# Performance work log

Measured on AMD Instinct MI355X. Metric: run time of the kernel, lower is better.

The kernel has to match this reference:

```python
import jax, jax.numpy as jnp
import numpy as np

B, L, IN = 8, 128, 64
H, C, A, HEADS = 800, 800, 128, 8
F = IN + H + 6          # states + inputs + angles(3) + distances(3)
RADIUS = 8.0
BOND = 3.8              # CA-CA virtual bond length (Angstrom)


def setup_inputs() -> dict:
    key = jax.random.key(0)
    ks = jax.random.split(key, 8)
    s = 0.05
    return {
        "data": jax.random.normal(ks[0], (B, L, IN), jnp.float32),
        # GRUCell (torch gate order r, z, n)
        "W_ih": jax.random.normal(ks[1], (IN + C, 3 * H), jnp.float32) * s,
        "W_hh": jax.random.normal(ks[2], (H, 3 * H), jnp.float32) * s,
        "b_ih": jnp.zeros((3 * H,), jnp.float32),
        "b_hh": jnp.zeros((3 * H,), jnp.float32),
        # AngleProject: hidden -> 3 torsion angles
        "Wa": jax.random.normal(ks[3], (H, 3), jnp.float32) * s,
        "ba": jnp.zeros((3,), jnp.float32),
        # MILAttention: tanh(x W1) W2 -> per-head logits; head-pooled feats -> context
        "W1": jax.random.normal(ks[4], (F, A), jnp.float32) * s,
        "b1": jnp.zeros((A,), jnp.float32),
        "W2": jax.random.normal(ks[5], (A, HEADS), jnp.float32) * s,
        "Wout": jax.random.normal(ks[6], (HEADS * F, C), jnp.float32) * s,
        "bout": jnp.zeros((C,), jnp.float32),
    }


def _gru(x, h, W_ih, W_hh, b_ih, b_hh):
    gx = x @ W_ih + b_ih
    gh = h @ W_hh + b_hh
    xr, xz, xn = jnp.split(gx, 3, axis=-1)
    hr, hz, hn = jnp.split(gh, 3, axis=-1)
    r = jax.nn.sigmoid(xr + hr)
    z = jax.nn.sigmoid(xz + hz)
    n = jnp.tanh(xn + r * hn)
    return (1.0 - z) * n + z * h


def _forward(data, W_ih, W_hh, b_ih, b_hh, Wa, ba, W1, b1, W2, Wout, bout):
    jpos = jnp.arange(L)

    def step(carry, idx):
        state, context, results, angles, positions = carry
        x = jnp.concatenate([data[:, idx, :], context], axis=-1)        # [B, IN+C]
        state = _gru(x, state, W_ih, W_hh, b_ih, b_hh)                  # [B, H]
        angle = state @ Wa + ba                                         # [B, 3]
        prev = jnp.where(idx > 0, positions[:, idx - 1], 0.0)           # [B, 3, 3]
        # LocalPositionLookup: extend backbone by BOND along angle-derived dirs
        asum = jnp.sum(angle, axis=-1, keepdims=True)
        dirs = jnp.stack([jnp.cos(angle),
                          jnp.sin(angle) * jnp.cos(asum),
                          jnp.sin(angle) * jnp.sin(asum)], axis=-1)     # [B, 3, 3]
        tert = prev + BOND * dirs
        results = results.at[:, idx].set(state)
        angles = angles.at[:, idx].set(angle)
        positions = positions.at[:, idx].set(tert)
        # collect_context: neighbors = {j < idx : ||CA_j - CA_{idx-1}|| <= radius}
        diff = prev[:, None, :, :] - positions                          # [B, L, 3, 3]
        dist = jnp.sqrt(jnp.sum(diff * diff, axis=-1) + 1e-12)          # [B, L, 3]
        mask = (jpos[None, :] < idx) & (dist[:, :, 1] <= RADIUS)        # [B, L]
        feats = jnp.concatenate([results, data, angles, dist], axis=-1)  # [B, L, F]
        # MIL attention pooling per chain (bag = neighbor set)
        e = jnp.tanh(feats @ W1 + b1)                                   # [B, L, A]
        logits = jnp.where(mask[:, :, None], e @ W2, -1e9)              # [B, L, HEADS]
        attn = jax.nn.softmax(logits, axis=1)
        pooled = jnp.einsum('blh,blf->bhf', attn, feats).reshape(B, HEADS * F)
        ctx = pooled @ Wout + bout                                      # [B, C]
        context = jnp.where(idx > 0, ctx, 0.0)
        return (state, context, results, angles, positions), None

    init = (jnp.zeros((B, H), jnp.float32),
            jnp.zeros((B, C), jnp.float32),
            jnp.zeros((B, L, H), jnp.float32),
            jnp.zeros((B, L, 3), jnp.float32),
            jnp.zeros((B, L, 3, 3), jnp.float32))
    (_, _, _, angles, positions), _ = jax.lax.scan(step, init, jnp.arange(L))
    return positions, angles


def reference(data, W_ih, W_hh, b_ih, b_hh, Wa, ba, W1, b1, W2, Wout, bout):
    return _forward(data, W_ih, W_hh, b_ih, b_hh, Wa, ba, W1, b1, W2, Wout, bout)
```

## Files before the change

### kernel.cpp

```cpp
#include <hip/hip_runtime.h>
#include <cmath>

namespace {

constexpr int B_ = 8, L_ = 128, IN_ = 64, H_ = 800, C_ = 800, A_ = 128, HD_ = 8;
constexpr int F_ = 870;
constexpr int KX_ = IN_ + C_;
constexpr int KO_ = HD_ * F_;
constexpr double RAD_ = 8.0, BOND_ = 3.8;
constexpr int NB = 256, NT = 512;

constexpr size_t OF_RES = 1024;
constexpr size_t OF_WIT = OF_RES + (size_t)B_ * L_ * H_;
constexpr size_t OF_WHT = OF_WIT + (size_t)3 * H_ * KX_;
constexpr size_t OF_WOT = OF_WHT + (size_t)3 * H_ * H_;
constexpr size_t FLT_END = OF_WOT + (size_t)C_ * KO_;
constexpr size_t D_ST  = 0;
constexpr size_t D_CTX = D_ST + 2ull * B_ * H_;
constexpr size_t D_ANG = D_CTX + (size_t)B_ * C_;
constexpr size_t D_POS = D_ANG + (size_t)B_ * L_ * 3;
constexpr size_t D_DST = D_POS + (size_t)B_ * L_ * 9;
constexpr size_t D_G   = D_DST + 2ull * B_ * L_ * 3;
constexpr size_t D_W   = D_G + (size_t)B_ * L_ * A_;
constexpr size_t D_PN  = D_W + (size_t)B_ * L_ * HD_;
constexpr size_t D_END = D_PN + (size_t)B_ * KO_;
constexpr size_t WS_BYTES = FLT_END * 4 + D_END * 8;

constexpr int LD_NEUR = 4992;
constexpr int LD_WOUT_A = 24960;
constexpr int LD_TOT = 38880;

__device__ __forceinline__ void gbar(unsigned* cnt, unsigned& ep) {
  ++ep;
  __syncthreads();
  const unsigned grp = (unsigned)blockIdx.x >> 5;
  if (threadIdx.x == 0)
    __hip_atomic_fetch_add(&cnt[32 + grp * 32], 1u,
                           __ATOMIC_RELEASE, __HIP_MEMORY_SCOPE_AGENT);
  if (blockIdx.x == 0) {
    if (threadIdx.x < 8) {
      const unsigned tgt = ep * 32u;
      while (__hip_atomic_load(&cnt[32 + threadIdx.x * 32],
                               __ATOMIC_RELAXED, __HIP_MEMORY_SCOPE_AGENT) < tgt)
        __builtin_amdgcn_s_sleep(1);
    }
    if (threadIdx.x == 0)
      __builtin_amdgcn_fence(__ATOMIC_ACQUIRE, "agent");
    __syncthreads();
    if (threadIdx.x < 8)
      __hip_atomic_store(&cnt[288 + threadIdx.x * 32], ep,
                         __ATOMIC_RELEASE, __HIP_MEMORY_SCOPE_AGENT);
    __syncthreads();
  } else {
    if (threadIdx.x == 0) {
      while (__hip_atomic_load(&cnt[288 + grp * 32],
                               __ATOMIC_RELAXED, __HIP_MEMORY_SCOPE_AGENT) < ep)
        __builtin_amdgcn_s_sleep(1);
      __builtin_amdgcn_fence(__ATOMIC_ACQUIRE, "agent");
    }
    __syncthreads();
  }
}

__device__ void transp(const float* __restrict__ src, float* __restrict__ dst,
                       int R, int Cn, float* sm) {
  const int tr_ = (R + 31) >> 5, tc_ = (Cn + 31) >> 5;
  for (int t = blockIdx.x; t < tr_ * tc_; t += gridDim.x) {
    const int r0 = (t / tc_) << 5, c0 = (t % tc_) << 5;
    __syncthreads();
    for (int e = threadIdx.x; e < 1024; e += NT) {
      const int rr = e >> 5, cc = e & 31, r = r0 + rr, c = c0 + cc;
      sm[rr * 33 + cc] = (r < R && c < Cn) ? src[(size_t)r * Cn + c] : 0.0f;
    }
    __syncthreads();
    for (int e = threadIdx.x; e < 1024; e += NT) {
      const int cc = e >> 5, rr = e & 5 * 0 + (e & 31), r = r0 + (e & 31), c = c0 + (e >> 5);
      (void)rr;
      if (r < R && c < Cn) dst[(size_t)c * R + r] = sm[(e & 31) * 33 + (e >> 5)];
    }
  }
}

}

extern "C" __global__ __launch_bounds__(NT, 1)
void srnn(const float* __restrict__ data, const float* __restrict__ W_ih,
          const float* __restrict__ W_hh, const float* __restrict__ b_ih,
          const float* __restrict__ b_hh, const float* __restrict__ Wa,
          const float* __restrict__ ba, const float* __restrict__ W1,
          const float* __restrict__ b1, const float* __restrict__ W2,
          const float* __restrict__ Wout, const float* __restrict__ bout,
          float* __restrict__ out, float* __restrict__ ws)
{
  __shared__ __align__(16) float wlds[LD_TOT];
  __shared__ double smd[528];
  float* smf = (float*)smd;
  unsigned* cnt = (unsigned*)ws;
  float* res   = ws + OF_RES;
  float* WihT  = ws + OF_WIT;
  float* WhhT  = ws + OF_WHT;
  float* WoutT = ws + OF_WOT;
  double* wd   = (double*)(ws + FLT_END);
  double* st2  = wd + D_ST;
  double* ctxD = wd + D_CTX;
  double* angD = wd + D_ANG;
  double* posD = wd + D_POS;
  double* dstD = wd + D_DST;
  double* Gd   = wd + D_G;
  double* wAr  = wd + D_W;
  double* pND  = wd + D_PN;

  const int bid = blockIdx.x, tid = threadIdx.x;
  const int wid = tid >> 6, lane = tid & 63;
  unsigned ep = 0;

  for (int i = bid * NT + tid; i < (int)(D_ANG - D_ST); i += NB * NT)
    wd[i] = 0.0;
  {
    const int i = bid * NT + tid;
    const int a = i & (A_ - 1);
    const int bj = i >> 7;
    double acc = (double)b1[a];
    const float* dr = data + (size_t)bj * IN_;
    #pragma unroll 8
    for (int k = 0; k < IN_; ++k)
      acc = fma((double)dr[k], (double)W1[(size_t)(H_ + k) * A_ + a], acc);
    Gd[i] = acc;
  }
  transp(W_ih, WihT, KX_, 3 * H_, smf);
  transp(W_hh, WhhT, H_, 3 * H_, smf);
  transp(Wout, WoutT, KO_, C_, smf);
  gbar(cnt, ep);

  if (bid < 160) {
    for (int rg = 0; rg < 15; ++rg) {
      const int s = rg / 3, g = rg % 3;
      const int i = bid * 5 + s;
      const float4* src = reinterpret_cast<const float4*>(WihT + (size_t)(g * H_ + i) * KX_);
      float4* dst = reinterpret_cast<float4*>(&wlds[s * LD_NEUR + g * 864]);
      for (int k4 = tid; k4 < 216; k4 += NT) dst[k4] = src[k4];
    }
    for (int rg = 0; rg < 15; ++rg) {
      const int s = rg / 3, g = rg % 3;
      const int i = bid * 5 + s;
      const float4* src = reinterpret_cast<const float4*>(WhhT + (size_t)(g * H_ + i) * H_);
      float4* dst = reinterpret_cast<float4*>(&wlds[s * LD_NEUR + 2592 + g * 800]);
      for (int k4 = tid; k4 < 200; k4 += NT) dst[k4] = src[k4];
    }
    for (int cs = 0; cs < 2; ++cs) {
      const int c = bid * 2 + cs;
      const float4* src = reinterpret_cast<const float4*>(WoutT + (size_t)c * KO_);
      float4* dst = reinterpret_cast<float4*>(&wlds[LD_WOUT_A + cs * KO_]);
      for (int k4 = tid; k4 < 1740; k4 += NT) dst[k4] = src[k4];
    }
  } else {
    for (int cs = 0; cs < 5; ++cs) {
      const int c = 320 + (bid - 160) * 5 + cs;
      const float4* src = reinterpret_cast<const float4*>(WoutT + (size_t)c * KO_);
      float4* dst = reinterpret_cast<float4*>(&wlds[cs * KO_]);
      for (int k4 = tid; k4 < 1740; k4 += NT) dst[k4] = src[k4];
    }
  }
  __syncthreads();

  for (int idx = 0; idx < L_; ++idx) {
    const int rp = idx & 1;
    const double* sOld = st2 + (size_t)rp * B_ * H_;
    double* sNew = st2 + (size_t)(rp ^ 1) * B_ * H_;
    const double* dstR = dstD + (size_t)(idx & 1) * (B_ * L_ * 3);
    double* dstW = dstD + (size_t)((idx + 1) & 1) * (B_ * L_ * 3);

    if (bid < 160 && wid < 5) {
      const int i = bid * 5 + wid;
      const int b = lane >> 3, ks = lane & 7;
      const float4* wr4 = reinterpret_cast<const float4*>(&wlds[wid * LD_NEUR]);
      const float4* wz4 = reinterpret_cast<const float4*>(&wlds[wid * LD_NEUR + 864]);
      const float4* wn4 = reinterpret_cast<const float4*>(&wlds[wid * LD_NEUR + 1728]);
      const float4* dx4 = reinterpret_cast<const float4*>(data + ((size_t)b * L_ + idx) * IN_);
      const double* cx = ctxD + (size_t)b * C_;
      double axr = 0., axz = 0., axn = 0.;
      #pragma unroll
      for (int j = 0; j < 2; ++j) {
        const int q = ks + 8 * j;
        const float4 x4 = dx4[q];
        const float4 r4 = wr4[q], z4 = wz4[q], n4 = wn4[q];
        const double x0 = x4.x, x1 = x4.y, x2 = x4.z, x3 = x4.w;
        axr = fma((double)r4.x, x0, axr); axr = fma((double)r4.y, x1, axr);
        axr = fma((double)r4.z, x2, axr); axr = fma((double)r4.w, x3, axr);
        axz = fma((double)z4.x, x0, axz); axz = fma((double)z4.y, x1, axz);
        axz = fma((double)z4.z, x2, axz); axz = fma((double)z4.w, x3, axz);
        axn = fma((double)n4.x, x0, axn); axn = fma((double)n4.y, x1, axn);
        axn = fma((double)n4.z, x2, axn); axn = fma((double)n4.w, x3, axn);
      }
      for (int j = 2; j < 27; ++j) {
        const int q = ks + 8 * j;
        const int e = 4 * q - 64;
        const double x0 = cx[e], x1 = cx[e + 1], x2 = cx[e + 2], x3 = cx[e + 3];
        const float4 r4 = wr4[q], z4 = wz4[q], n4 = wn4[q];
        axr = fma((double)r4.x, x0, axr); axr = fma((double)r4.y, x1, axr);
        axr = fma((double)r4.z, x2, axr); axr = fma((double)r4.w, x3, axr);
        axz = fma((double)z4.x, x0, axz); axz = fma((double)z4.y, x1, axz);
        axz = fma((double)z4.z, x2, axz); axz = fma((double)z4.w, x3, axz);
        axn = fma((double)n4.x, x0, axn); axn = fma((double)n4.y, x1, axn);
        axn = fma((double)n4.z, x2, axn); axn = fma((double)n4.w, x3, axn);
      }
      const float4* hr4 = reinterpret_cast<const float4*>(&wlds[wid * LD_NEUR + 2592]);
      const float4* hz4 = reinterpret_cast<const float4*>(&wlds[wid * LD_NEUR + 2592 + 800]);
      const float4* hn4 = reinterpret_cast<const float4*>(&wlds[wid * LD_NEUR + 2592 + 1600]);
      const double* sx = sOld + (size_t)b * H_;
      double ahr = 0., ahz = 0., ahn = 0.;
      for (int j = 0; j < 25; ++j) {
        const int q = ks + 8 * j;
        const int e = 4 * q;
        const double s0 = sx[e], s1 = sx[e + 1], s2 = sx[e + 2], s3 = sx[e + 3];
        const float4 r4 = hr4[q], z4 = hz4[q], n4 = hn4[q];
        ahr = fma((double)r4.x, s0, ahr); ahr = fma((double)r4.y, s1, ahr);
        ahr = fma((double)r4.z, s2, ahr); ahr = fma((double)r4.w, s3, ahr);
        ahz = fma((double)z4.x, s0, ahz); ahz = fma((double)z4.y, s1, ahz);
        ahz = fma((double)z4.z, s2, ahz); ahz = fma((double)z4.w, s3, ahz);
        ahn = fma((double)n4.x, s0, ahn); ahn = fma((double)n4.y, s1, ahn);
        ahn = fma((double)n4.z, s2, ahn); ahn = fma((double)n4.w, s3, ahn);
      }
      #pragma unroll
      for (int off = 1; off < 8; off <<= 1) {
        axr += __shfl_xor(axr, off); axz += __shfl_xor(axz, off); axn += __shfl_xor(axn, off);
        ahr += __shfl_xor(ahr, off); ahz += __shfl_xor(ahz, off); ahn += __shfl_xor(ahn, off);
      }
      if (ks == 0) {
        const double xr = axr + (double)b_ih[i], xz = axz + (double)b_ih[H_ + i],
                     xn = axn + (double)b_ih[2 * H_ + i];
        const double hr = ahr + (double)b_hh[i], hz = ahz + (double)b_hh[H_ + i],
                     hn = ahn + (double)b_hh[2 * H_ + i];
        const double r = 1.0 / (1.0 + exp(-(xr + hr)));
        const double z = 1.0 / (1.0 + exp(-(xz + hz)));
        const double n = tanh(xn + r * hn);
        const double sn = (1.0 - z) * n + z * sOld[b * H_ + i];
        sNew[b * H_ + i] = sn;
        res[((size_t)b * L_ + idx) * H_ + i] = (float)sn;
      }
    } else {
      int tsk = -1;
      if (bid >= 160) tsk = (bid - 160) * 8 + wid;
      else tsk = 768 + bid * 3 + (wid - 5);
      if (tsk < 1024 && idx > 0) {
        const int b = tsk >> 7, j = tsk & (L_ - 1);
        const size_t bj = (size_t)b * L_ + j;
        double e0 = Gd[bj * A_ + lane], e1 = Gd[bj * A_ + lane + 64];
        const double an0 = angD[bj * 3], an1 = angD[bj * 3 + 1], an2 = angD[bj * 3 + 2];
        const double dd0 = dstR[bj * 3], dd1 = dstR[bj * 3 + 1], dd2 = dstR[bj * 3 + 2];
        e0 = fma((double)W1[864 * A_ + lane], an0, e0);
        e0 = fma((double)W1[865 * A_ + lane], an1, e0);
        e0 = fma((double)W1[866 * A_ + lane], an2, e0);
        e0 = fma((double)W1[867 * A_ + lane], dd0, e0);
        e0 = fma((double)W1[868 * A_ + lane], dd1, e0);
        e0 = fma((double)W1[869 * A_ + lane], dd2, e0);
        e1 = fma((double)W1[864 * A_ + lane + 64], an0, e1);
        e1 = fma((double)W1[865 * A_ + lane + 64], an1, e1);
        e1 = fma((double)W1[866 * A_ + lane + 64], an2, e1);
        e1 = fma((double)W1[867 * A_ + lane + 64], dd0, e1);
        e1 = fma((double)W1[868 * A_ + lane + 64], dd1, e1);
        e1 = fma((double)W1[869 * A_ + lane + 64], dd2, e1);
        e0 = tanh(e0); e1 = tanh(e1);
        double lg[8];
        #pragma unroll
        for (int h = 0; h < 8; ++h) {
          double v = fma(e0, (double)W2[lane * 8 + h], e1 * (double)W2[(lane + 64) * 8 + h]);
          #pragma unroll
          for (int off = 1; off < 64; off <<= 1) v += __shfl_xor(v, off);
          lg[h] = v;
        }
        if (lane == 0) {
          const bool valid = (j < idx) && (dd1 <= RAD_);
          double* wrow = wAr + bj * HD_;
          #pragma unroll
          for (int h = 0; h < 8; ++h) wrow[h] = valid ? exp(lg[h]) : 0.0;
        }
      }
    }
    gbar(cnt, ep);

    if (bid < 128) {
      if (idx > 0) {
        const int b = bid >> 4, sl = bid & 15;
        const int f0 = sl * 55;
        const int fn = (F_ - f0 < 55) ? (F_ - f0) : 55;
        const int fl = tid >> 3, h = tid & 7;
        if (fl < fn) {
          const int f = f0 + fl;
          const float* fbf = nullptr; const double* fbd = nullptr; int strd = 0;
          if (f < H_)                { fbf = res  + f + (size_t)b * L_ * H_;               strd = H_;  }
          else if (f < H_ + IN_)     { fbf = data + (f - H_) + (size_t)b * L_ * IN_;       strd = IN_; }
          else if (f < H_ + IN_ + 3) { fbd = angD + (f - H_ - IN_) + (size_t)b * L_ * 3;   strd = 3;   }
          else                       { fbd = dstR + (f - H_ - IN_ - 3) + (size_t)b * L_ * 3; strd = 3; }
          const double* wp = wAr + (size_t)b * L_ * HD_ + h;
          double acc = 0.0, zs = 0.0;
          for (int j = 0; j < idx; ++j) {
            const double wj = wp[(size_t)j * HD_];
            zs += wj;
            const double fv = fbf ? (double)fbf[(size_t)j * strd] : fbd[(size_t)j * strd];
            acc = fma(wj, fv, acc);
          }
          pND[(size_t)b * KO_ + (size_t)h * F_ + f] = acc / zs;
        }
      }
    } else if (bid < 136) {
      const int b = bid - 128;
      const int a = tid & (A_ - 1), ksl = tid >> 7;
      const double* sr = sNew + (size_t)b * H_;
      const int i0 = ksl * 200;
      double p = 0.0;
      for (int k = 0; k < 200; ++k)
        p = fma(sr[i0 + k], (double)W1[(size_t)(i0 + k) * A_ + a], p);
      smd[tid] = p;
      __syncthreads();
      if (tid < 128)
        Gd[((size_t)b * L_ + idx) * A_ + tid] +=
            smd[tid] + smd[128 + tid] + smd[256 + tid] + smd[384 + tid];
    } else if (bid == 136) {
      const int b7 = tid / 48, rem = tid % 48, t3 = rem / 16, ksl = rem & 15;
      if (tid < 384) {
        const double* sr = sNew + (size_t)b7 * H_;
        const int i0 = ksl * 50;
        double p = 0.0;
        for (int k = 0; k < 50; ++k)
          p = fma(sr[i0 + k], (double)Wa[(i0 + k) * 3 + t3], p);
        smd[tid] = p;
      }
      __syncthreads();
      if (tid < 24) {
        const int b2 = tid / 3, t4 = tid % 3;
        double s = (double)ba[t4];
        for (int u = 0; u < 16; ++u) s += smd[b2 * 48 + t4 * 16 + u];
        smd[384 + tid] = s;
        angD[((size_t)b2 * L_ + idx) * 3 + t4] = s;
        out[(size_t)B_ * L_ * 9 + ((size_t)b2 * L_ + idx) * 3 + t4] = (float)s;
      }
      __syncthreads();
      if (tid < 24) {
        const int b2 = tid / 3, t4 = tid % 3;
        const double a = smd[384 + b2 * 3 + t4];
        const double asum = smd[384 + b2 * 3] + smd[384 + b2 * 3 + 1] + smd[384 + b2 * 3 + 2];
        const double sa = sin(a), ca = cos(a), cs = cos(asum), ss = sin(asum);
        double px = 0., py = 0., pz = 0.;
        if (idx > 0) {
          const double* pr = posD + ((size_t)b2 * L_ + idx - 1) * 9 + t4 * 3;
          px = pr[0]; py = pr[1]; pz = pr[2];
        }
        px = fma(BOND_, ca, px);
        py = fma(BOND_, sa * cs, py);
        pz = fma(BOND_, sa * ss, pz);
        double* pw = posD + ((size_t)b2 * L_ + idx) * 9 + t4 * 3;
        pw[0] = px; pw[1] = py; pw[2] = pz;
        float* ow = out + ((size_t)b2 * L_ + idx) * 9 + t4 * 3;
        ow[0] = (float)px; ow[1] = (float)py; ow[2] = (float)pz;
      }
      __syncthreads();
      if (idx < L_ - 1) {
        for (int u = tid; u < 4096; u += NT) {
          const int b = u >> 9, rem2 = u & 511;
          const int j = rem2 >> 2, t6 = rem2 & 3;
          if (t6 < 3 && j <= idx) {
            const double* pa = posD + ((size_t)b * L_ + idx) * 9 + t6 * 3;
            const double* pb = posD + ((size_t)b * L_ + j) * 9 + t6 * 3;
            const double dx = pa[0] - pb[0], dy = pa[1] - pb[1], dz = pa[2] - pb[2];
            dstW[((size_t)b * L_ + j) * 3 + t6] =
                sqrt(fma(dx, dx, fma(dy, dy, fma(dz, dz, 1e-12))));
          }
        }
      }
    }
    gbar(cnt, ep);

    if (idx < L_ - 1) {
      const int ntask = (bid < 160) ? 2 : 5;
      for (int u = 0; u < ntask; ++u) {
        const int t = wid + 8 * u;
        const int cs = t >> 3, b = t & 7;
        const int c = (bid < 160) ? (bid * 2 + cs) : (320 + (bid - 160) * 5 + cs);
        const int cbase = ((bid < 160) ? LD_WOUT_A : 0) + cs * KO_;
        double acc = 0.0;
        if (idx > 0) {
          const double* pr = pND + (size_t)b * KO_;
          for (int m = 0; m < 28; ++m) {
            const int q = lane + 64 * m;
            if (q < 1740) {
              const float4 w4 = *reinterpret_cast<const float4*>(&wlds[cbase + 4 * q]);
              const int e = 4 * q;
              acc = fma((double)w4.x, pr[e],     acc);
              acc = fma((double)w4.y, pr[e + 1], acc);
              acc = fma((double)w4.z, pr[e + 2], acc);
              acc = fma((double)w4.w, pr[e + 3], acc);
            }
          }
          #pragma unroll
          for (int off = 1; off < 64; off <<= 1) acc += __shfl_xor(acc, off);
        }
        if (lane == 0)
          ctxD[b * C_ + c] = (idx > 0) ? (acc + (double)bout[c]) : 0.0;
      }
    }
    gbar(cnt, ep);
  }
}

extern "C" void kernel_launch(void* const* d_in, const int* in_sizes, int n_in,
                              void* d_out, int out_size, void* d_ws, size_t ws_size,
                              hipStream_t stream) {
  (void)in_sizes; (void)n_in; (void)out_size;
  if (ws_size < WS_BYTES) return;
  const float* data = (const float*)d_in[0];
  const float* W_ih = (const float*)d_in[1];
  const float* W_hh = (const float*)d_in[2];
  const float* b_ih = (const float*)d_in[3];
  const float* b_hh = (const float*)d_in[4];
  const float* Wa   = (const float*)d_in[5];
  const float* ba   = (const float*)d_in[6];
  const float* W1   = (const float*)d_in[7];
  const float* b1   = (const float*)d_in[8];
  const float* W2   = (const float*)d_in[9];
  const float* Wout = (const float*)d_in[10];
  const float* bout = (const float*)d_in[11];
  hipMemsetAsync(d_ws, 0, 4096, stream);
  srnn<<<dim3(NB), dim3(NT), 0, stream>>>(data, W_ih, W_hh, b_ih, b_hh, Wa, ba,
                                          W1, b1, W2, Wout, bout,
                                          (float*)d_out, (float*)d_ws);
}
```

Baseline: 12.71 ms.

## Use XCC-hierarchical grid barrier and load weights directly without global transpose

Replaces the centralized block-0 grid barrier in the time loop with a two-level barrier. Blocks count arrivals per XCC (read from a hardware register), and the last arriver on each XCC bumps one global counter that everyone polls. This removes the serial relay through block 0 at each of the three barriers per step. It also drops the global-memory transposes of W_ih, W_hh and Wout, gathering columns straight into LDS with strided loads instead, and skips attention-logit work for rows j >= idx. The strided gather may be less coalesced, and the barrier depends on the XCC id register and on counts of blocks per XCC.

```diff
diff --git a/kernel.cpp b/kernel.cpp
--- a/kernel.cpp
+++ b/kernel.cpp
@@ -10,11 +10,8 @@
 constexpr double RAD_ = 8.0, BOND_ = 3.8;
 constexpr int NB = 256, NT = 512;
 
-constexpr size_t OF_RES = 1024;
-constexpr size_t OF_WIT = OF_RES + (size_t)B_ * L_ * H_;
-constexpr size_t OF_WHT = OF_WIT + (size_t)3 * H_ * KX_;
-constexpr size_t OF_WOT = OF_WHT + (size_t)3 * H_ * H_;
-constexpr size_t FLT_END = OF_WOT + (size_t)C_ * KO_;
+constexpr size_t OF_RES = 2048;
+constexpr size_t FLT_END = OF_RES + (size_t)B_ * L_ * H_;
 constexpr size_t D_ST  = 0;
 constexpr size_t D_CTX = D_ST + 2ull * B_ * H_;
 constexpr size_t D_ANG = D_CTX + (size_t)B_ * C_;
@@ -30,55 +27,54 @@
 constexpr int LD_WOUT_A = 24960;
 constexpr int LD_TOT = 38880;
 
-__device__ __forceinline__ void gbar(unsigned* cnt, unsigned& ep) {
-  ++ep;
+__device__ __forceinline__ void gbar_init(unsigned* cnt) {
   __syncthreads();
   const unsigned grp = (unsigned)blockIdx.x >> 5;
   if (threadIdx.x == 0)
-    __hip_atomic_fetch_add(&cnt[32 + grp * 32], 1u,
+    __hip_atomic_fetch_add(&cnt[(24 + grp) * 32], 1u,
                            __ATOMIC_RELEASE, __HIP_MEMORY_SCOPE_AGENT);
   if (blockIdx.x == 0) {
     if (threadIdx.x < 8) {
-      const unsigned tgt = ep * 32u;
-      while (__hip_atomic_load(&cnt[32 + threadIdx.x * 32],
-                               __ATOMIC_RELAXED, __HIP_MEMORY_SCOPE_AGENT) < tgt)
-        __builtin_amdgcn_s_sleep(1);
+      while (__hip_atomic_load(&cnt[(24 + threadIdx.x) * 32],
+                               __ATOMIC_RELAXED, __HIP_MEMORY_SCOPE_AGENT) < 32u)
+        __builtin_amdgcn_s_sleep(8);
     }
     if (threadIdx.x == 0)
       __builtin_amdgcn_fence(__ATOMIC_ACQUIRE, "agent");
     __syncthreads();
     if (threadIdx.x < 8)
-      __hip_atomic_store(&cnt[288 + threadIdx.x * 32], ep,
+      __hip_atomic_store(&cnt[(32 + threadIdx.x) * 32], 1u,
                          __ATOMIC_RELEASE, __HIP_MEMORY_SCOPE_AGENT);
     __syncthreads();
   } else {
     if (threadIdx.x == 0) {
-      while (__hip_atomic_load(&cnt[288 + grp * 32],
-                               __ATOMIC_RELAXED, __HIP_MEMORY_SCOPE_AGENT) < ep)
-        __builtin_amdgcn_s_sleep(1);
+      while (__hip_atomic_load(&cnt[(32 + grp) * 32],
+                               __ATOMIC_RELAXED, __HIP_MEMORY_SCOPE_AGENT) < 1u)
+        __builtin_amdgcn_s_sleep(8);
       __builtin_amdgcn_fence(__ATOMIC_ACQUIRE, "agent");
     }
     __syncthreads();
   }
 }
 
-__device__ void transp(const float* __restrict__ src, float* __restrict__ dst,
-                       int R, int Cn, float* sm) {
-  const int tr_ = (R + 31) >> 5, tc_ = (Cn + 31) >> 5;
-  for (int t = blockIdx.x; t < tr_ * tc_; t += gridDim.x) {
-    const int r0 = (t / tc_) << 5, c0 = (t % tc_) << 5;
-    __syncthreads();
-    for (int e = threadIdx.x; e < 1024; e += NT) {
-      const int rr = e >> 5, cc = e & 31, r = r0 + rr, c = c0 + cc;
-      sm[rr * 33 + cc] = (r < R && c < Cn) ? src[(size_t)r * Cn + c] : 0.0f;
-    }
-    __syncthreads();
-    for (int e = threadIdx.x; e < 1024; e += NT) {
-      const int cc = e >> 5, rr = e & 5 * 0 + (e & 31), r = r0 + (e & 31), c = c0 + (e >> 5);
-      (void)rr;
-      if (r < R && c < Cn) dst[(size_t)c * R + r] = sm[(e & 31) * 33 + (e >> 5)];
-    }
-  }
+__device__ __forceinline__ void gbarx(unsigned* cnt, unsigned& ep,
+                                      unsigned xcc, unsigned xcnt, unsigned nx) {
+  ++ep;
+  __syncthreads();
+  if (threadIdx.x == 0) {
+    const unsigned old = __hip_atomic_fetch_add(&cnt[xcc * 32], 1u,
+                             __ATOMIC_RELAXED, __HIP_MEMORY_SCOPE_AGENT);
+    if (old == ep * xcnt - 1u) {
+      __builtin_amdgcn_fence(__ATOMIC_RELEASE, "agent");
+      __hip_atomic_fetch_add(&cnt[256], 1u,
+                             __ATOMIC_RELAXED, __HIP_MEMORY_SCOPE_AGENT);
+    }
+    while (__hip_atomic_load(&cnt[256],
+                             __ATOMIC_RELAXED, __HIP_MEMORY_SCOPE_AGENT) < ep * nx)
+      __builtin_amdgcn_s_sleep(8);
+    __builtin_amdgcn_fence(__ATOMIC_ACQUIRE, "agent");
+  }
+  __syncthreads();
 }
 
 }
@@ -94,12 +90,9 @@
 {
   __shared__ __align__(16) float wlds[LD_TOT];
   __shared__ double smd[528];
-  float* smf = (float*)smd;
+  __shared__ unsigned s_xcc, s_xcnt, s_nx;
   unsigned* cnt = (unsigned*)ws;
   float* res   = ws + OF_RES;
-  float* WihT  = ws + OF_WIT;
-  float* WhhT  = ws + OF_WHT;
-  float* WoutT = ws + OF_WOT;
   double* wd   = (double*)(ws + FLT_END);
   double* st2  = wd + D_ST;
   double* ctxD = wd + D_CTX;
@@ -113,6 +106,15 @@
   const int bid = blockIdx.x, tid = threadIdx.x;
   const int wid = tid >> 6, lane = tid & 63;
   unsigned ep = 0;
+
+  if (tid == 0) {
+    unsigned x;
+    asm volatile("s_getreg_b32 %0, hwreg(HW_REG_XCC_ID)" : "=s"(x));
+    x &= 7u;
+    s_xcc = x;
+    __hip_atomic_fetch_add(&cnt[(16 + x) * 32], 1u,
+                           __ATOMIC_RELAXED, __HIP_MEMORY_SCOPE_AGENT);
+  }
 
   for (int i = bid * NT + tid; i < (int)(D_ANG - D_ST); i += NB * NT)
     wd[i] = 0.0;
@@ -127,41 +129,40 @@
       acc = fma((double)dr[k], (double)W1[(size_t)(H_ + k) * A_ + a], acc);
     Gd[i] = acc;
   }
-  transp(W_ih, WihT, KX_, 3 * H_, smf);
-  transp(W_hh, WhhT, H_, 3 * H_, smf);
-  transp(Wout, WoutT, KO_, C_, smf);
-  gbar(cnt, ep);
-
   if (bid < 160) {
-    for (int rg = 0; rg < 15; ++rg) {
-      const int s = rg / 3, g = rg % 3;
-      const int i = bid * 5 + s;
-      const float4* src = reinterpret_cast<const float4*>(WihT + (size_t)(g * H_ + i) * KX_);
-      float4* dst = reinterpret_cast<float4*>(&wlds[s * LD_NEUR + g * 864]);
-      for (int k4 = tid; k4 < 216; k4 += NT) dst[k4] = src[k4];
-    }
-    for (int rg = 0; rg < 15; ++rg) {
-      const int s = rg / 3, g = rg % 3;
-      const int i = bid * 5 + s;
-      const float4* src = reinterpret_cast<const float4*>(WhhT + (size_t)(g * H_ + i) * H_);
-      float4* dst = reinterpret_cast<float4*>(&wlds[s * LD_NEUR + 2592 + g * 800]);
-      for (int k4 = tid; k4 < 200; k4 += NT) dst[k4] = src[k4];
-    }
-    for (int cs = 0; cs < 2; ++cs) {
-      const int c = bid * 2 + cs;
-      const float4* src = reinterpret_cast<const float4*>(WoutT + (size_t)c * KO_);
-      float4* dst = reinterpret_cast<float4*>(&wlds[LD_WOUT_A + cs * KO_]);
-      for (int k4 = tid; k4 < 1740; k4 += NT) dst[k4] = src[k4];
+    for (int e = tid; e < 5 * 3 * 864; e += NT) {
+      const int s = e / 2592, rem = e % 2592, g = rem / 864, k = rem % 864;
+      wlds[s * LD_NEUR + g * 864 + k] =
+          W_ih[(size_t)k * (3 * H_) + g * H_ + bid * 5 + s];
+    }
+    for (int e = tid; e < 5 * 3 * 800; e += NT) {
+      const int s = e / 2400, rem = e % 2400, g = rem / 800, k = rem % 800;
+      wlds[s * LD_NEUR + 2592 + g * 800 + k] =
+          W_hh[(size_t)k * (3 * H_) + g * H_ + bid * 5 + s];
+    }
+    for (int e = tid; e < 2 * KO_; e += NT) {
+      const int cs = e / KO_, k = e % KO_;
+      wlds[LD_WOUT_A + cs * KO_ + k] = Wout[(size_t)k * C_ + bid * 2 + cs];
     }
   } else {
-    for (int cs = 0; cs < 5; ++cs) {
-      const int c = 320 + (bid - 160) * 5 + cs;
-      const float4* src = reinterpret_cast<const float4*>(WoutT + (size_t)c * KO_);
-      float4* dst = reinterpret_cast<float4*>(&wlds[cs * KO_]);
-      for (int k4 = tid; k4 < 1740; k4 += NT) dst[k4] = src[k4];
-    }
+    for (int e = tid; e < 5 * KO_; e += NT) {
+      const int cs = e / KO_, k = e % KO_;
+      wlds[cs * KO_ + k] = Wout[(size_t)k * C_ + 320 + (bid - 160) * 5 + cs];
+    }
+  }
+  gbar_init(cnt);
+
+  if (tid == 0) {
+    unsigned n = 0;
+    for (int k = 0; k < 8; ++k)
+      n += (__hip_atomic_load(&cnt[(16 + k) * 32],
+                              __ATOMIC_RELAXED, __HIP_MEMORY_SCOPE_AGENT) > 0u);
+    s_nx = n;
+    s_xcnt = __hip_atomic_load(&cnt[(16 + s_xcc) * 32],
+                               __ATOMIC_RELAXED, __HIP_MEMORY_SCOPE_AGENT);
   }
   __syncthreads();
+  const unsigned xcc = s_xcc, xcnt = s_xcnt, nx = s_nx;
 
   for (int idx = 0; idx < L_; ++idx) {
     const int rp = idx & 1;
@@ -244,40 +245,42 @@
       else tsk = 768 + bid * 3 + (wid - 5);
       if (tsk < 1024 && idx > 0) {
         const int b = tsk >> 7, j = tsk & (L_ - 1);
-        const size_t bj = (size_t)b * L_ + j;
-        double e0 = Gd[bj * A_ + lane], e1 = Gd[bj * A_ + lane + 64];
-        const double an0 = angD[bj * 3], an1 = angD[bj * 3 + 1], an2 = angD[bj * 3 + 2];
-        const double dd0 = dstR[bj * 3], dd1 = dstR[bj * 3 + 1], dd2 = dstR[bj * 3 + 2];
-        e0 = fma((double)W1[864 * A_ + lane], an0, e0);
-        e0 = fma((double)W1[865 * A_ + lane], an1, e0);
-        e0 = fma((double)W1[866 * A_ + lane], an2, e0);
-        e0 = fma((double)W1[867 * A_ + lane], dd0, e0);
-        e0 = fma((double)W1[868 * A_ + lane], dd1, e0);
-        e0 = fma((double)W1[869 * A_ + lane], dd2, e0);
-        e1 = fma((double)W1[864 * A_ + lane + 64], an0, e1);
-        e1 = fma((double)W1[865 * A_ + lane + 64], an1, e1);
-        e1 = fma((double)W1[866 * A_ + lane + 64], an2, e1);
-        e1 = fma((double)W1[867 * A_ + lane + 64], dd0, e1);
-        e1 = fma((double)W1[868 * A_ + lane + 64], dd1, e1);
-        e1 = fma((double)W1[869 * A_ + lane + 64], dd2, e1);
-        e0 = tanh(e0); e1 = tanh(e1);
-        double lg[8];
-        #pragma unroll
-        for (int h = 0; h < 8; ++h) {
-          double v = fma(e0, (double)W2[lane * 8 + h], e1 * (double)W2[(lane + 64) * 8 + h]);
+        if (j < idx) {
+          const size_t bj = (size_t)b * L_ + j;
+          double e0 = Gd[bj * A_ + lane], e1 = Gd[bj * A_ + lane + 64];
+          const double an0 = angD[bj * 3], an1 = angD[bj * 3 + 1], an2 = angD[bj * 3 + 2];
+          const double dd0 = dstR[bj * 3], dd1 = dstR[bj * 3 + 1], dd2 = dstR[bj * 3 + 2];
+          e0 = fma((double)W1[864 * A_ + lane], an0, e0);
+          e0 = fma((double)W1[865 * A_ + lane], an1, e0);
+          e0 = fma((double)W1[866 * A_ + lane], an2, e0);
+          e0 = fma((double)W1[867 * A_ + lane], dd0, e0);
+          e0 = fma((double)W1[868 * A_ + lane], dd1, e0);
+          e0 = fma((double)W1[869 * A_ + lane], dd2, e0);
+          e1 = fma((double)W1[864 * A_ + lane + 64], an0, e1);
+          e1 = fma((double)W1[865 * A_ + lane + 64], an1, e1);
+          e1 = fma((double)W1[866 * A_ + lane + 64], an2, e1);
+          e1 = fma((double)W1[867 * A_ + lane + 64], dd0, e1);
+          e1 = fma((double)W1[868 * A_ + lane + 64], dd1, e1);
+          e1 = fma((double)W1[869 * A_ + lane + 64], dd2, e1);
+          e0 = tanh(e0); e1 = tanh(e1);
+          double lg[8];
           #pragma unroll
-          for (int off = 1; off < 64; off <<= 1) v += __shfl_xor(v, off);
-          lg[h] = v;
+          for (int h = 0; h < 8; ++h) {
+            double v = fma(e0, (double)W2[lane * 8 + h], e1 * (double)W2[(lane + 64) * 8 + h]);
+            #pragma unroll
+            for (int off = 1; off < 64; off <<= 1) v += __shfl_xor(v, off);
+            lg[h] = v;
+          }
+          if (lane == 0) {
+            const bool valid = (dd1 <= RAD_);
+            double* wrow = wAr + bj * HD_;
+            #pragma unroll
+            for (int h = 0; h < 8; ++h) wrow[h] = valid ? exp(lg[h]) : 0.0;
+          }
         }
-        if (lane == 0) {
-          const bool valid = (j < idx) && (dd1 <= RAD_);
-          double* wrow = wAr + bj * HD_;
-          #pragma unroll
-          for (int h = 0; h < 8; ++h) wrow[h] = valid ? exp(lg[h]) : 0.0;
-        }
-      }
-    }
-    gbar(cnt, ep);
+      }
+    }
+    gbarx(cnt, ep, xcc, xcnt, nx);
 
     if (bid < 128) {
       if (idx > 0) {
@@ -369,7 +372,7 @@
         }
       }
     }
-    gbar(cnt, ep);
+    gbarx(cnt, ep, xcc, xcnt, nx);
 
     if (idx < L_ - 1) {
       const int ntask = (bid < 160) ? 2 : 5;
@@ -399,7 +402,7 @@
           ctxD[b * C_ + c] = (idx > 0) ? (acc + (double)bout[c]) : 0.0;
       }
     }
-    gbar(cnt, ep);
+    gbarx(cnt, ep, xcc, xcnt, nx);
   }
 }
 
@@ -420,7 +423,7 @@
   const float* W2   = (const float*)d_in[9];
   const float* Wout = (const float*)d_in[10];
   const float* bout = (const float*)d_in[11];
-  hipMemsetAsync(d_ws, 0, 4096, stream);
+  hipMemsetAsync(d_ws, 0, 8192, stream);
   srnn<<<dim3(NB), dim3(NT), 0, stream>>>(data, W_ih, W_hh, b_ih, b_hh, Wa, ba,
                                           W1, b1, W2, Wout, bout,
                                           (float*)d_out, (float*)d_ws);
```

New measurement: 11.38 ms. -10.5%, faster.
